# Kernel tuning notes

Measured on AMD Instinct MI355X. Metric: run time of the kernel, lower is better.

Reference implementation:

```python
import jax, jax.numpy as jnp
import numpy as np
from jax import lax

IH, IW = 32, 32
N = IH * IW
C = 256
HEADS = 8
DH = C // HEADS
SCALE = 32 ** -0.5  # uses dim_head arg (32), as in the torch module
EPS = 1e-6


def _rel_index():
    coords = np.stack(np.meshgrid(np.arange(IH), np.arange(IW), indexing='ij')).reshape(2, -1)
    rel = coords[:, :, None] - coords[:, None, :]  # [2, n, n]
    rel[0] += IH - 1
    rel[1] += IW - 1
    rel[0] *= 2 * IW - 1
    return jnp.asarray(rel.sum(0).reshape(-1))  # [n*n] int

REL_IDX = _rel_index()


def _conv3(x, W):
    # 3x3 conv, stride 1, pad 1, no bias; NCHW / OIHW
    return lax.conv_general_dilated(x, W, (1, 1), 'SAME',
                                    dimension_numbers=('NCHW', 'OIHW', 'NCHW'))


def _proj(x, W, g, b):
    # conv3x3 -> GroupNorm(1 group, per-channel affine) -> exact GELU -> split heads
    y = _conv3(x, W)
    m = jnp.mean(y, axis=(1, 2, 3), keepdims=True)
    v = jnp.var(y, axis=(1, 2, 3), keepdims=True)
    y = (y - m) * lax.rsqrt(v + EPS) * g[None, :, None, None] + b[None, :, None, None]
    y = jax.nn.gelu(y, approximate=False)
    B = y.shape[0]
    # b c h w -> b (h d heads split) : channel c = head*DH + d  -> b h n d
    return y.reshape(B, HEADS, DH, N).transpose(0, 1, 3, 2)


def setup_inputs() -> dict:
    key = jax.random.key(0)
    ks = jax.random.split(key, 8)
    s = 0.02
    return {
        'x': jax.random.normal(ks[0], (8, C, IH, IW), dtype=jnp.float32),
        'Wq': jax.random.normal(ks[1], (C, C, 3, 3), dtype=jnp.float32) * s,
        'gq': jnp.ones((C,), jnp.float32), 'bq': jnp.zeros((C,), jnp.float32),
        'Wk': jax.random.normal(ks[2], (C, C, 3, 3), dtype=jnp.float32) * s,
        'gk': jnp.ones((C,), jnp.float32), 'bk': jnp.zeros((C,), jnp.float32),
        'Wv': jax.random.normal(ks[3], (C, C, 3, 3), dtype=jnp.float32) * s,
        'gv': jnp.ones((C,), jnp.float32), 'bv': jnp.zeros((C,), jnp.float32),
        'bias_table': jax.random.normal(ks[4], ((2 * IH - 1) * (2 * IW - 1), HEADS), dtype=jnp.float32) * s,
        'Wout': jax.random.normal(ks[5], (C, C, 1, 1), dtype=jnp.float32) * s,
        'bout': jnp.zeros((C,), jnp.float32),
    }


def reference(x, Wq, gq, bq, Wk, gk, bk, Wv, gv, bv, bias_table, Wout, bout):
    B = x.shape[0]
    q = _proj(x, Wq, gq, bq)  # [B, H, N, DH]
    k = _proj(x, Wk, gk, bk)
    v = _proj(x, Wv, gv, bv)
    dots = jnp.einsum('bhnd,bhmd->bhnm', q, k) * SCALE  # [B, H, N, N]
    # gather relative position bias: [n*n, heads] -> [1, heads, n, n]
    bias = bias_table[REL_IDX].reshape(N, N, HEADS).transpose(2, 0, 1)[None]
    attn = jax.nn.softmax(dots + bias, axis=-1)
    out = jnp.einsum('bhnm,bhmd->bhnd', attn, v)  # [B, H, N, DH]
    # b h n d -> b n (h d) -> b c ih iw
    out = out.transpose(0, 2, 1, 3).reshape(B, N, C).transpose(0, 2, 1).reshape(B, C, IH, IW)
    # 1x1 conv projection with bias (Dropout2d is identity at eval)
    out = jnp.einsum('oc,bchw->bohw', Wout[:, :, 0, 0], out) + bout[None, :, None, None]
    return out
```

## Files before the change

### kernel.cpp

```cpp
#include <hip/hip_runtime.h>

typedef float f32x4 __attribute__((ext_vector_type(4)));
typedef short bf16x8 __attribute__((ext_vector_type(8)));
typedef short bf16x4 __attribute__((ext_vector_type(4)));

#define PADN 1156

typedef const __attribute__((address_space(1))) void* gptr_t;
typedef __attribute__((address_space(3))) void* lptr_t;

__device__ __forceinline__ short f2b(float f) {
  unsigned u = __float_as_uint(f);
  unsigned r = (u + 0x7FFFu + ((u >> 16) & 1u)) >> 16;
  return (short)r;
}
__device__ __forceinline__ float b2f(short s) {
  return __uint_as_float(((unsigned)(unsigned short)s) << 16);
}

__global__ __launch_bounds__(256) void prep(const float* __restrict__ x,
                                            const float* __restrict__ Wq,
                                            const float* __restrict__ Wk,
                                            const float* __restrict__ Wv,
                                            const float* __restrict__ Wout,
                                            short* __restrict__ xpad,
                                            short* __restrict__ wpack,
                                            short* __restrict__ woutp,
                                            float* __restrict__ stats) {
  __shared__ float lds[2304];
  int blk0 = blockIdx.x;
  int t = threadIdx.x;
  if (blk0 < 2048) {
    int wg = blk0;
    int b = wg >> 8, rem = wg & 255;
    int cb = rem >> 5, sb = rem & 31;
    int sl = t & 31, cq = t >> 5;
    const float* xb = x + ((b * 256 + cb * 32) * 1024) + sb * 32;
#pragma unroll
    for (int i = 0; i < 4; i++) {
      int cl = cq + i * 8;
      lds[cl * 33 + sl] = xb[cl * 1024 + sl];
    }
    __syncthreads();
    int cl2 = t & 31, sq = t >> 5;
    short* xp = xpad + b * (PADN * 256) + cb * 32 + cl2;
#pragma unroll
    for (int i = 0; i < 4; i++) {
      int sl2 = sq + i * 8;
      int s = sb * 32 + sl2;
      int pidx = ((s >> 5) + 1) * 34 + (s & 31) + 1;
      xp[pidx * 256] = f2b(lds[cl2 * 33 + sl2]);
    }
  } else if (blk0 < 2880) {
    int blk = blk0 - 2048;
    if (blk < 768) {
      int p = blk >> 8, o = blk & 255;
      const float* W = (p == 0) ? Wq : (p == 1) ? Wk : Wv;
      const float* src = W + o * 2304;
      for (int i = t; i < 2304; i += 256) lds[i] = src[i];
      __syncthreads();
      short* dst = wpack + p * 589824 + o * 2304;
#pragma unroll
      for (int tt = 0; tt < 9; tt++) dst[tt * 256 + t] = f2b(lds[t * 9 + tt]);
    } else {
      int e = (blk - 768) * 1024 + t * 4;
      f32x4 v = *(const f32x4*)(Wout + e);
      bf16x4 o4;
#pragma unroll
      for (int j = 0; j < 4; j++) o4[j] = f2b(v[j]);
      *(bf16x4*)(woutp + e) = o4;
    }
  } else if (blk0 < 3012) {
    int id = (blk0 - 2880) * 256 + t;
    int chunk = id & 31;
    int r2 = id >> 5;
    int pos = r2 % 132;
    int b = r2 / 132;
    int pidx;
    if (pos < 34) pidx = pos;
    else if (pos < 68) pidx = 1122 + (pos - 34);
    else if (pos < 100) pidx = (pos - 67) * 34;
    else pidx = (pos - 99) * 34 + 33;
    bf16x8 z = {};
    *(bf16x8*)(xpad + (size_t)b * (PADN * 256) + pidx * 256 + chunk * 8) = z;
  } else {
    if (t < 64) stats[t] = 0.f;
  }
}

__global__ __launch_bounds__(256, 2) void conv_gemm(const short* __restrict__ xpad,
                                                    const short* __restrict__ wpack,
                                                    short* __restrict__ qn,
                                                    short* __restrict__ kn,
                                                    short* __restrict__ vn,
                                                    float* __restrict__ stats,
                                                    const float* __restrict__ btab,
                                                    short* __restrict__ biasP) {
  __shared__ short ldsA[2][8192];
  __shared__ short ldsB[2][8192];
  int bid = blockIdx.x;
  int tid = threadIdx.x;
  if (bid >= 384) {
    const float L2E = 1.4426950408889634f;
#pragma unroll
    for (int it = 0; it < 4; it++) {
      int id = (bid - 384) * 1024 + it * 256 + tid;
      int lane = id & 63;
      int rest = id >> 6;
      int jt = rest & 3; rest >>= 2;
      int kb = rest & 15; rest >>= 4;
      int qblk = rest & 63; rest >>= 6;
      int h = rest;
      int li = lane & 15, g = lane >> 4;
      int qrow = qblk * 16 + li;
      int yi = qrow >> 5, xi = qrow & 31;
      int ibase = (yi + 31) * 63 + (xi + 31);
      int j0 = kb * 64 + jt * 16 + g * 4;
      int yj = j0 >> 5, xj0 = j0 & 31;
      int idx0 = ibase - yj * 63 - xj0;
      bf16x4 v;
#pragma unroll
      for (int rr = 0; rr < 4; rr++) v[rr] = f2b(btab[(idx0 - rr) * 8 + h] * L2E);
      *(bf16x4*)(biasP + (size_t)id * 4) = v;
    }
    return;
  }
  int wg = (bid & 7) * 48 + (bid >> 3);
  int b = wg / 48;
  int rr0 = wg - b * 48;
  int p = (rr0 < 16) ? 0 : (rr0 < 32) ? 1 : 2;
  int t16 = rr0 & 15;
  bool xA = (p < 2);
  int mt_i = xA ? (t16 >> 1) : (t16 >> 3);
  int nt_i = xA ? (t16 & 1) : (t16 & 7);
  int m0 = mt_i * 128, n0 = nt_i * 128;
  int lane = tid & 63, wave = tid >> 6;
  int wr = wave >> 1, wc = wave & 1;
  int g = lane >> 4, li = lane & 15;

  const char* xb = (const char*)(xpad + b * (PADN * 256));
  const char* wp = (const char*)(wpack + p * (256 * 2304));
  const char* abase = xA ? xb : wp;
  const char* bbase = xA ? wp : xb;

  int srow = tid >> 3;
  int schunk = ((tid & 7) ^ (srow & 7)) * 16;
  int aoff[4], boff[4];
#pragma unroll
  for (int q = 0; q < 4; q++) {
    int row = m0 + q * 32 + srow;
    aoff[q] = (xA ? ((((row >> 5) + 1) * 34 + (row & 31) + 1) * 512) : (row * 4608)) + schunk;
  }
#pragma unroll
  for (int q = 0; q < 4; q++) {
    int row = n0 + q * 32 + srow;
    boff[q] = (xA ? (row * 4608) : ((((row >> 5) + 1) * 34 + (row & 31) + 1) * 512)) + schunk;
  }

  int aadr[4][2], badr[4][2];
#pragma unroll
  for (int mt = 0; mt < 4; mt++) {
    int row = wr * 64 + mt * 16 + li;
#pragma unroll
    for (int ksub = 0; ksub < 2; ksub++)
      aadr[mt][ksub] = row * 64 + (((ksub * 4 + g) ^ (row & 7)) * 8);
  }
#pragma unroll
  for (int nt = 0; nt < 4; nt++) {
    int row = wc * 64 + nt * 16 + li;
#pragma unroll
    for (int ksub = 0; ksub < 2; ksub++)
      badr[nt][ksub] = row * 64 + (((ksub * 4 + g) ^ (row & 7)) * 8);
  }

#define STAGE(KS, BUF) do {                                                        \
    int t_ = (KS) >> 2, cq_ = (KS) & 3;                                            \
    int ty_ = (t_ * 11) >> 5;                                                      \
    int doff_ = (ty_ - 1) * 34 + (t_ - 3 * ty_) - 1;                               \
    int kA_ = (xA ? doff_ * 512 : t_ * 512) + cq_ * 128;                           \
    int kB_ = (xA ? t_ * 512 : doff_ * 512) + cq_ * 128;                           \
    _Pragma("unroll")                                                              \
    for (int q_ = 0; q_ < 4; q_++)                                                 \
      __builtin_amdgcn_global_load_lds((gptr_t)(abase + aoff[q_] + kA_),           \
                                       (lptr_t)&ldsA[BUF][(q_ * 256 + tid) * 8],   \
                                       16, 0, 0);                                  \
    _Pragma("unroll")                                                              \
    for (int q_ = 0; q_ < 4; q_++)                                                 \
      __builtin_amdgcn_global_load_lds((gptr_t)(bbase + boff[q_] + kB_),           \
                                       (lptr_t)&ldsB[BUF][(q_ * 256 + tid) * 8],   \
                                       16, 0, 0);                                  \
  } while (0)

  f32x4 acc[4][4] = {};
  STAGE(0, 0);
  __syncthreads();
#pragma unroll 2
  for (int ks = 0; ks < 36; ks++) {
    int cur = ks & 1;
    if (ks < 35) STAGE(ks + 1, cur ^ 1);
    bf16x8 af[4][2], bfv[4][2];
#pragma unroll
    for (int mt = 0; mt < 4; mt++)
#pragma unroll
      for (int ksub = 0; ksub < 2; ksub++)
        af[mt][ksub] = *(const bf16x8*)&ldsA[cur][aadr[mt][ksub]];
#pragma unroll
    for (int nt = 0; nt < 4; nt++)
#pragma unroll
      for (int ksub = 0; ksub < 2; ksub++)
        bfv[nt][ksub] = *(const bf16x8*)&ldsB[cur][badr[nt][ksub]];
#pragma unroll
    for (int ksub = 0; ksub < 2; ksub++)
#pragma unroll
      for (int mt = 0; mt < 4; mt++)
#pragma unroll
        for (int nt = 0; nt < 4; nt++)
          acc[mt][nt] = __builtin_amdgcn_mfma_f32_16x16x32_bf16(af[mt][ksub], bfv[nt][ksub], acc[mt][nt], 0, 0, 0);
    __syncthreads();
  }
#undef STAGE

  short* outp = (p == 0) ? qn : (p == 1) ? kn : vn;
  int ostride = xA ? 256 : 1024;
  int obase = b * 262144;
  float s1 = 0.f, s2 = 0.f;
#pragma unroll
  for (int mt = 0; mt < 4; mt++)
#pragma unroll
    for (int nt = 0; nt < 4; nt++) {
      int col = n0 + wc * 64 + nt * 16 + li;
#pragma unroll
      for (int rr = 0; rr < 4; rr++) {
        int row = m0 + wr * 64 + mt * 16 + g * 4 + rr;
        float v = acc[mt][nt][rr];
        s1 += v;
        s2 += v * v;
        outp[obase + row * ostride + col] = f2b(v);
      }
    }
#pragma unroll
  for (int off = 1; off < 64; off <<= 1) {
    s1 += __shfl_xor(s1, off);
    s2 += __shfl_xor(s2, off);
  }
  if (lane == 0) {
    atomicAdd(&stats[(b * 3 + p) * 2], s1);
    atomicAdd(&stats[(b * 3 + p) * 2 + 1], s2);
  }
}

__global__ __launch_bounds__(256) void norm_gelu(const short* __restrict__ qn, const short* __restrict__ kn,
                                                 const short* __restrict__ vn,
                                                 short* __restrict__ qpk, short* __restrict__ kpk,
                                                 short* __restrict__ vpk,
                                                 const float* __restrict__ stats,
                                                 const float* __restrict__ gq, const float* __restrict__ bq,
                                                 const float* __restrict__ gk, const float* __restrict__ bk,
                                                 const float* __restrict__ gv, const float* __restrict__ bv) {
  long e = ((long)blockIdx.x * 256 + threadIdx.x) * 8;
  int buf = (int)(e >> 21);
  int w = (int)(e & 2097151);
  int b = w >> 18;
  int pos = w & 262143;
  const short* base = (buf == 0) ? qn : (buf == 1) ? kn : vn;
  const float* gg = (buf == 0) ? gq : (buf == 1) ? gk : gv;
  const float* bb = (buf == 0) ? bq : (buf == 1) ? bk : bv;
  float s1 = stats[(b * 3 + buf) * 2];
  float s2 = stats[(b * 3 + buf) * 2 + 1];
  float mean = s1 * (1.f / 262144.f);
  float var = s2 * (1.f / 262144.f) - mean * mean;
  float rstd = rsqrtf(var + 1e-6f);
  const float PS = 0.17677669529663687f * 1.4426950408889634f;
  float post = (buf == 0) ? PS : 1.f;
  bf16x8 v = *(const bf16x8*)(base + (size_t)b * 262144 + pos);
#pragma unroll
  for (int j = 0; j < 8; j++) {
    int ch = (buf < 2) ? ((pos + j) & 255) : ((pos + j) >> 10);
    float y = b2f(v[j]);
    y = (y - mean) * rstd * gg[ch] + bb[ch];
    y = 0.5f * y * (1.f + erff(y * 0.70710678118f));
    v[j] = f2b(y * post);
  }
  if (buf < 2) {
    int s = pos >> 8, c = pos & 255;
    int h2 = c >> 5, g2 = (c >> 3) & 3;
    short* dst = (buf == 0) ? qpk : kpk;
    size_t addr = ((size_t)((b * 8 + h2) * 64 + (s >> 4))) * 512 + (g2 * 16 + (s & 15)) * 8;
    *(bf16x8*)(dst + addr) = v;
  } else {
    int c = pos >> 10, s0 = pos & 1023;
    int h2 = c >> 5, d = c & 31;
    int dblk = d >> 4, liv = d & 15;
    int kv32 = s0 >> 5, jr0 = s0 & 31;
    int hi = jr0 >> 4, g0 = (jr0 >> 2) & 3;
    size_t addr = ((size_t)((b * 8 + h2) * 32 + kv32) * 2 + dblk) * 512 + hi * 4 + liv * 8;
    bf16x4 lo4 = {v[0], v[1], v[2], v[3]};
    bf16x4 hi4 = {v[4], v[5], v[6], v[7]};
    *(bf16x4*)(vpk + addr + g0 * 128) = lo4;
    *(bf16x4*)(vpk + addr + (g0 + 1) * 128) = hi4;
  }
}

__global__ __launch_bounds__(256, 4) void attn(const short* __restrict__ qpk,
                                               const short* __restrict__ kpk,
                                               const short* __restrict__ vpk,
                                               const short* __restrict__ biasP,
                                               short* __restrict__ obuf) {
  __shared__ short ldsK[2][2048];
  __shared__ short ldsV[2][2048];
  int wg = blockIdx.x;
  int b = wg >> 7, rem = wg & 127;
  int h = rem >> 4, qt4 = rem & 15;
  int tid = threadIdx.x;
  int lane = tid & 63, wave = tid >> 6;
  int g = lane >> 4, li = lane & 15;
  int qblk = qt4 * 4 + wave;
  int qbase = qblk * 16;
  const short* qpb = qpk + ((size_t)((b * 8 + h) * 64 + qblk)) * 512;
  const char* kpc = (const char*)(kpk + ((size_t)((b * 8 + h) * 64)) * 512);
  const char* vpc = (const char*)(vpk + ((size_t)(b * 8 + h)) * 32768);
  const short* bpb = biasP + (((size_t)(h * 64 + qblk)) << 14) + lane * 4;
  bf16x8 qf = *(const bf16x8*)(qpb + lane * 8);
  float m = -1e30f, l = 0.f;
  f32x4 oacc[2] = {};
  bf16x4 bfr[4];
#pragma unroll
  for (int jt = 0; jt < 4; jt++) bfr[jt] = *(const bf16x4*)(bpb + jt * 256);
  __builtin_amdgcn_global_load_lds((gptr_t)(kpc + tid * 16), (lptr_t)&ldsK[0][tid * 8], 16, 0, 0);
  __builtin_amdgcn_global_load_lds((gptr_t)(vpc + tid * 16), (lptr_t)&ldsV[0][tid * 8], 16, 0, 0);
  __syncthreads();
#pragma unroll 1
  for (int kb = 0; kb < 16; kb++) {
    int cur = kb & 1;
    if (kb < 15) {
      __builtin_amdgcn_global_load_lds((gptr_t)(kpc + (kb + 1) * 4096 + tid * 16),
                                       (lptr_t)&ldsK[cur ^ 1][tid * 8], 16, 0, 0);
      __builtin_amdgcn_global_load_lds((gptr_t)(vpc + (kb + 1) * 4096 + tid * 16),
                                       (lptr_t)&ldsV[cur ^ 1][tid * 8], 16, 0, 0);
    }
    f32x4 st[4];
    __builtin_amdgcn_s_setprio(1);
#pragma unroll
    for (int jt = 0; jt < 4; jt++) {
      bf16x8 kf = *(const bf16x8*)&ldsK[cur][jt * 512 + lane * 8];
      f32x4 cinit;
#pragma unroll
      for (int rr = 0; rr < 4; rr++) cinit[rr] = b2f(bfr[jt][rr]);
      st[jt] = __builtin_amdgcn_mfma_f32_16x16x32_bf16(kf, qf, cinit, 0, 0, 0);
    }
    __builtin_amdgcn_s_setprio(0);
    bf16x4 bfr2[4];
    if (kb < 15) {
#pragma unroll
      for (int jt = 0; jt < 4; jt++)
        bfr2[jt] = *(const bf16x4*)(bpb + (kb + 1) * 1024 + jt * 256);
    }
    float mbl = -1e30f;
#pragma unroll
    for (int jt = 0; jt < 4; jt++)
#pragma unroll
      for (int rr = 0; rr < 4; rr++) mbl = fmaxf(mbl, st[jt][rr]);
    if (!__all(mbl <= m + 8.f)) {
      float mb = fmaxf(mbl, __shfl_xor(mbl, 16));
      mb = fmaxf(mb, __shfl_xor(mb, 32));
      float mnew = fmaxf(m, mb);
      float alpha = exp2f(m - mnew);
      m = mnew;
      l *= alpha;
#pragma unroll
      for (int rr = 0; rr < 4; rr++) {
        float ar = __shfl(alpha, (lane & 0x30) | (g * 4 + rr));
        oacc[0][rr] *= ar;
        oacc[1][rr] *= ar;
      }
    }
    float ls = 0.f;
    bf16x8 pf0, pf1;
#pragma unroll
    for (int jt = 0; jt < 4; jt++)
#pragma unroll
      for (int rr = 0; rr < 4; rr++) {
        float pe = exp2f(st[jt][rr] - m);
        ls += pe;
        int q2 = jt * 4 + rr;
        if (q2 < 8) pf0[q2] = f2b(pe); else pf1[q2 - 8] = f2b(pe);
      }
    l += ls;
    __builtin_amdgcn_s_setprio(1);
#pragma unroll
    for (int nt = 0; nt < 2; nt++)
#pragma unroll
      for (int ks = 0; ks < 2; ks++) {
        bf16x8 vf = *(const bf16x8*)&ldsV[cur][(ks * 2 + nt) * 512 + lane * 8];
        oacc[nt] = __builtin_amdgcn_mfma_f32_16x16x32_bf16(ks == 0 ? pf0 : pf1, vf, oacc[nt], 0, 0, 0);
      }
    __builtin_amdgcn_s_setprio(0);
    if (kb < 15) {
#pragma unroll
      for (int jt = 0; jt < 4; jt++) bfr[jt] = bfr2[jt];
    }
    __syncthreads();
  }
  l += __shfl_xor(l, 16);
  l += __shfl_xor(l, 32);
  float linv = 1.f / l;
  short* ob = obuf + (b * 1024) * 256 + h * 32;
#pragma unroll
  for (int rr = 0; rr < 4; rr++) {
    float lr = __shfl(linv, (lane & 0x30) | (g * 4 + rr));
    int row = qbase + g * 4 + rr;
    ob[row * 256 + li] = f2b(oacc[0][rr] * lr);
    ob[row * 256 + 16 + li] = f2b(oacc[1][rr] * lr);
  }
}

__global__ __launch_bounds__(256) void out_gemm(const short* __restrict__ woutp,
                                                const short* __restrict__ obuf,
                                                const float* __restrict__ bout,
                                                float* __restrict__ out) {
  int wg = blockIdx.x;
  int b = wg >> 5, rem = wg & 31;
  int mt_i = rem >> 4, nt_i = rem & 15;
  int m0 = mt_i * 128, n0 = nt_i * 64;
  int lane = threadIdx.x & 63, wave = threadIdx.x >> 6;
  int wr = wave >> 1, wc = wave & 1;
  int g = lane >> 4, li = lane & 15;
  int aoff[4];
#pragma unroll
  for (int mt = 0; mt < 4; mt++) aoff[mt] = (m0 + wr * 64 + mt * 16 + li) * 256;
  int boff[2];
#pragma unroll
  for (int nt = 0; nt < 2; nt++) boff[nt] = (b * 1024 + n0 + wc * 32 + nt * 16 + li) * 256;
  f32x4 acc[4][2] = {};
#pragma unroll
  for (int ks = 0; ks < 8; ks++) {
    int kof = ks * 32 + g * 8;
    bf16x8 af[4], bfr[2];
#pragma unroll
    for (int mt = 0; mt < 4; mt++) af[mt] = *(const bf16x8*)(woutp + aoff[mt] + kof);
#pragma unroll
    for (int nt = 0; nt < 2; nt++) bfr[nt] = *(const bf16x8*)(obuf + boff[nt] + kof);
#pragma unroll
    for (int mt = 0; mt < 4; mt++)
#pragma unroll
      for (int nt = 0; nt < 2; nt++)
        acc[mt][nt] = __builtin_amdgcn_mfma_f32_16x16x32_bf16(af[mt], bfr[nt], acc[mt][nt], 0, 0, 0);
  }
#pragma unroll
  for (int mt = 0; mt < 4; mt++)
#pragma unroll
    for (int nt = 0; nt < 2; nt++) {
      int col = n0 + wc * 32 + nt * 16 + li;
#pragma unroll
      for (int rr = 0; rr < 4; rr++) {
        int row = m0 + wr * 64 + mt * 16 + g * 4 + rr;
        out[b * 262144 + row * 1024 + col] = acc[mt][nt][rr] + bout[row];
      }
    }
}

extern "C" void kernel_launch(void* const* d_in, const int* in_sizes, int n_in,
                              void* d_out, int out_size, void* d_ws, size_t ws_size,
                              hipStream_t stream) {
  const float* x = (const float*)d_in[0];
  const float* Wq = (const float*)d_in[1];
  const float* gq = (const float*)d_in[2];
  const float* bq = (const float*)d_in[3];
  const float* Wk = (const float*)d_in[4];
  const float* gk = (const float*)d_in[5];
  const float* bk = (const float*)d_in[6];
  const float* Wv = (const float*)d_in[7];
  const float* gv = (const float*)d_in[8];
  const float* bv = (const float*)d_in[9];
  const float* btab = (const float*)d_in[10];
  const float* Wout = (const float*)d_in[11];
  const float* bout = (const float*)d_in[12];
  float* out = (float*)d_out;

  char* ws = (char*)d_ws;
  size_t off = 0;
  float* stats = (float*)(ws + off); off += 256;
  short* xpad = (short*)(ws + off); off += (size_t)8 * PADN * 256 * 2;
  short* wpack = (short*)(ws + off); off += (size_t)3 * 256 * 2304 * 2;
  short* woutp = (short*)(ws + off); off += (size_t)256 * 256 * 2;
  short* qn = (short*)(ws + off); off += (size_t)4194304;
  short* kn = (short*)(ws + off); off += (size_t)4194304;
  short* vn = (short*)(ws + off); off += (size_t)4194304;
  short* obuf = (short*)(ws + off); off += (size_t)4194304;
  short* qpk = (short*)(ws + off); off += (size_t)4194304;
  short* kpk = (short*)(ws + off); off += (size_t)4194304;
  short* vpk = (short*)(ws + off); off += (size_t)4194304;
  short* biasP = (short*)(ws + off); off += (size_t)8 * 1024 * 1024 * 2;
  if (ws_size < off) return;

  prep<<<3013, 256, 0, stream>>>(x, Wq, Wk, Wv, Wout, xpad, wpack, woutp, stats);
  conv_gemm<<<2432, 256, 0, stream>>>(xpad, wpack, qn, kn, vn, stats, btab, biasP);
  norm_gelu<<<3072, 256, 0, stream>>>(qn, kn, vn, qpk, kpk, vpk, stats, gq, bq, gk, bk, gv, bv);
  attn<<<1024, 256, 0, stream>>>(qpk, kpk, vpk, biasP, obuf);
  out_gemm<<<256, 256, 0, stream>>>(woutp, obuf, bout, out);
}
```

Before: 139.5 us.

## Split conv GEMM K dimension in two and reduce via fp32 atomics

The conv GEMM's 36-step K loop is split into two halves, doubling the tile blocks from 384 to 768 to fill more CUs. Partial sums are accumulated with fp32 atomicAdd into a zero-initialized fp32 buffer, so statistics move to a new statsred kernel that rereads that buffer. norm_gelu now reads fp32 instead of bf16. This adds zeroing work, scattered atomic traffic, double the intermediate memory and an extra launch in exchange for better occupancy of the largest GEMM.

```diff
diff --git a/kernel.cpp b/kernel.cpp
--- a/kernel.cpp
+++ b/kernel.cpp
@@ -26,7 +26,8 @@
                                             short* __restrict__ xpad,
                                             short* __restrict__ wpack,
                                             short* __restrict__ woutp,
-                                            float* __restrict__ stats) {
+                                            float* __restrict__ stats,
+                                            float* __restrict__ pbuf) {
   __shared__ float lds[2304];
   int blk0 = blockIdx.x;
   int t = threadIdx.x;
@@ -83,28 +84,30 @@
     else pidx = (pos - 99) * 34 + 33;
     bf16x8 z = {};
     *(bf16x8*)(xpad + (size_t)b * (PADN * 256) + pidx * 256 + chunk * 8) = z;
+  } else if (blk0 == 3012) {
+    if (t < 64) stats[t] = 0.f;
   } else {
-    if (t < 64) stats[t] = 0.f;
+    float* dst = pbuf + (size_t)(blk0 - 3013) * 4096 + t * 4;
+    f32x4 z = {};
+#pragma unroll
+    for (int i = 0; i < 4; i++) *(f32x4*)(dst + i * 1024) = z;
   }
 }
 
 __global__ __launch_bounds__(256, 2) void conv_gemm(const short* __restrict__ xpad,
                                                     const short* __restrict__ wpack,
-                                                    short* __restrict__ qn,
-                                                    short* __restrict__ kn,
-                                                    short* __restrict__ vn,
-                                                    float* __restrict__ stats,
+                                                    float* __restrict__ pbuf,
                                                     const float* __restrict__ btab,
                                                     short* __restrict__ biasP) {
   __shared__ short ldsA[2][8192];
   __shared__ short ldsB[2][8192];
   int bid = blockIdx.x;
   int tid = threadIdx.x;
-  if (bid >= 384) {
+  if (bid >= 768) {
     const float L2E = 1.4426950408889634f;
 #pragma unroll
     for (int it = 0; it < 4; it++) {
-      int id = (bid - 384) * 1024 + it * 256 + tid;
+      int id = (bid - 768) * 1024 + it * 256 + tid;
       int lane = id & 63;
       int rest = id >> 6;
       int jt = rest & 3; rest >>= 2;
@@ -125,7 +128,10 @@
     }
     return;
   }
-  int wg = (bid & 7) * 48 + (bid >> 3);
+  int half = (bid >= 384) ? 1 : 0;
+  int tile = bid - half * 384;
+  int ks0 = half * 18, ks1 = ks0 + 18;
+  int wg = (tile & 7) * 48 + (tile >> 3);
   int b = wg / 48;
   int rr0 = wg - b * 48;
   int p = (rr0 < 16) ? 0 : (rr0 < 32) ? 1 : 2;
@@ -192,12 +198,12 @@
   } while (0)
 
   f32x4 acc[4][4] = {};
-  STAGE(0, 0);
+  STAGE(ks0, 0);
   __syncthreads();
 #pragma unroll 2
-  for (int ks = 0; ks < 36; ks++) {
-    int cur = ks & 1;
-    if (ks < 35) STAGE(ks + 1, cur ^ 1);
+  for (int ks = ks0; ks < ks1; ks++) {
+    int cur = (ks - ks0) & 1;
+    if (ks < ks1 - 1) STAGE(ks + 1, cur ^ 1);
     bf16x8 af[4][2], bfv[4][2];
 #pragma unroll
     for (int mt = 0; mt < 4; mt++)
@@ -220,10 +226,8 @@
   }
 #undef STAGE
 
-  short* outp = (p == 0) ? qn : (p == 1) ? kn : vn;
+  float* outp = pbuf + (size_t)p * 2097152 + (size_t)b * 262144;
   int ostride = xA ? 256 : 1024;
-  int obase = b * 262144;
-  float s1 = 0.f, s2 = 0.f;
 #pragma unroll
   for (int mt = 0; mt < 4; mt++)
 #pragma unroll
@@ -232,25 +236,40 @@
 #pragma unroll
       for (int rr = 0; rr < 4; rr++) {
         int row = m0 + wr * 64 + mt * 16 + g * 4 + rr;
-        float v = acc[mt][nt][rr];
-        s1 += v;
-        s2 += v * v;
-        outp[obase + row * ostride + col] = f2b(v);
+        atomicAdd(&outp[row * ostride + col], acc[mt][nt][rr]);
       }
     }
+}
+
+__global__ __launch_bounds__(256) void statsred(const float* __restrict__ pbuf,
+                                                float* __restrict__ stats) {
+  int blk = blockIdx.x;
+  int tid = threadIdx.x;
+  int p = blk >> 9;
+  int b = (blk & 511) >> 6;
+  const float* src = pbuf + (size_t)blk * 4096;
+  float s1 = 0.f, s2 = 0.f;
+#pragma unroll
+  for (int i = 0; i < 4; i++) {
+    f32x4 v = *(const f32x4*)(src + i * 1024 + tid * 4);
+#pragma unroll
+    for (int j = 0; j < 4; j++) {
+      s1 += v[j];
+      s2 += v[j] * v[j];
+    }
+  }
 #pragma unroll
   for (int off = 1; off < 64; off <<= 1) {
     s1 += __shfl_xor(s1, off);
     s2 += __shfl_xor(s2, off);
   }
-  if (lane == 0) {
+  if ((tid & 63) == 0) {
     atomicAdd(&stats[(b * 3 + p) * 2], s1);
     atomicAdd(&stats[(b * 3 + p) * 2 + 1], s2);
   }
 }
 
-__global__ __launch_bounds__(256) void norm_gelu(const short* __restrict__ qn, const short* __restrict__ kn,
-                                                 const short* __restrict__ vn,
+__global__ __launch_bounds__(256) void norm_gelu(const float* __restrict__ pbuf,
                                                  short* __restrict__ qpk, short* __restrict__ kpk,
                                                  short* __restrict__ vpk,
                                                  const float* __restrict__ stats,
@@ -262,7 +281,7 @@
   int w = (int)(e & 2097151);
   int b = w >> 18;
   int pos = w & 262143;
-  const short* base = (buf == 0) ? qn : (buf == 1) ? kn : vn;
+  const float* base = pbuf + (size_t)buf * 2097152 + (size_t)b * 262144 + pos;
   const float* gg = (buf == 0) ? gq : (buf == 1) ? gk : gv;
   const float* bb = (buf == 0) ? bq : (buf == 1) ? bk : bv;
   float s1 = stats[(b * 3 + buf) * 2];
@@ -272,11 +291,13 @@
   float rstd = rsqrtf(var + 1e-6f);
   const float PS = 0.17677669529663687f * 1.4426950408889634f;
   float post = (buf == 0) ? PS : 1.f;
-  bf16x8 v = *(const bf16x8*)(base + (size_t)b * 262144 + pos);
+  f32x4 v0 = *(const f32x4*)(base);
+  f32x4 v1 = *(const f32x4*)(base + 4);
+  bf16x8 v;
 #pragma unroll
   for (int j = 0; j < 8; j++) {
     int ch = (buf < 2) ? ((pos + j) & 255) : ((pos + j) >> 10);
-    float y = b2f(v[j]);
+    float y = (j < 4) ? v0[j] : v1[j - 4];
     y = (y - mean) * rstd * gg[ch] + bb[ch];
     y = 0.5f * y * (1.f + erff(y * 0.70710678118f));
     v[j] = f2b(y * post);
@@ -483,9 +504,7 @@
   short* xpad = (short*)(ws + off); off += (size_t)8 * PADN * 256 * 2;
   short* wpack = (short*)(ws + off); off += (size_t)3 * 256 * 2304 * 2;
   short* woutp = (short*)(ws + off); off += (size_t)256 * 256 * 2;
-  short* qn = (short*)(ws + off); off += (size_t)4194304;
-  short* kn = (short*)(ws + off); off += (size_t)4194304;
-  short* vn = (short*)(ws + off); off += (size_t)4194304;
+  float* pbuf = (float*)(ws + off); off += (size_t)6291456 * 4;
   short* obuf = (short*)(ws + off); off += (size_t)4194304;
   short* qpk = (short*)(ws + off); off += (size_t)4194304;
   short* kpk = (short*)(ws + off); off += (size_t)4194304;
@@ -493,9 +512,10 @@
   short* biasP = (short*)(ws + off); off += (size_t)8 * 1024 * 1024 * 2;
   if (ws_size < off) return;
 
-  prep<<<3013, 256, 0, stream>>>(x, Wq, Wk, Wv, Wout, xpad, wpack, woutp, stats);
-  conv_gemm<<<2432, 256, 0, stream>>>(xpad, wpack, qn, kn, vn, stats, btab, biasP);
-  norm_gelu<<<3072, 256, 0, stream>>>(qn, kn, vn, qpk, kpk, vpk, stats, gq, bq, gk, bk, gv, bv);
+  prep<<<4549, 256, 0, stream>>>(x, Wq, Wk, Wv, Wout, xpad, wpack, woutp, stats, pbuf);
+  conv_gemm<<<2816, 256, 0, stream>>>(xpad, wpack, pbuf, btab, biasP);
+  statsred<<<1536, 256, 0, stream>>>(pbuf, stats);
+  norm_gelu<<<3072, 256, 0, stream>>>(pbuf, qpk, kpk, vpk, stats, gq, bq, gk, bk, gv, bv);
   attn<<<1024, 256, 0, stream>>>(qpk, kpk, vpk, biasP, obuf);
   out_gemm<<<256, 256, 0, stream>>>(woutp, obuf, bout, out);
 }
```

New measurement: 235.8 us. +69.0%, slower.
